# Kernel tuning notes

Measured on AMD Instinct MI355X. Metric: run time of the kernel, lower is better.

## Reference

```python
import jax, jax.numpy as jnp
import numpy as np

NEG = -1e30  # effective -inf that stays stable in fp32 log-sum-exp
BLANK = 0


def _lse3(a, b, c):
    m = jnp.maximum(jnp.maximum(a, b), c)
    return m + jnp.log(jnp.exp(a - m) + jnp.exp(b - m) + jnp.exp(c - m))


def _ctc_loss_sum(log_probs, input_lengths, targets, target_lengths):
    # log_probs: [B, T, V] already log-softmaxed; targets: [B, S] int, blank=0
    B, T, V = log_probs.shape
    S = targets.shape[1]
    L = 2 * S + 1  # extended label seq: blank-interleaved

    ext = jnp.full((B, L), BLANK, dtype=targets.dtype)
    ext = ext.at[:, 1::2].set(targets)  # [B, L]

    # gather per-frame log-probs of extended labels: [B, T, L]
    lp_ext = jnp.take_along_axis(
        log_probs, jnp.broadcast_to(ext[:, None, :], (B, T, L)), axis=2)

    # skip transition s-2 -> s allowed iff ext[s] != blank and ext[s] != ext[s-2]
    ext_prev2 = jnp.pad(ext[:, :-2], ((0, 0), (2, 0)), constant_values=BLANK)
    can_skip = (ext != BLANK) & (ext != ext_prev2) & (jnp.arange(L)[None, :] >= 2)

    # alpha init at t=0
    alpha = jnp.full((B, L), NEG, dtype=log_probs.dtype)
    alpha = alpha.at[:, 0].set(lp_ext[:, 0, 0])
    alpha = alpha.at[:, 1].set(lp_ext[:, 0, 1])

    lp_seq = jnp.swapaxes(lp_ext, 0, 1)[1:]          # [T-1, B, L]
    valid = jnp.arange(1, T)[:, None] < input_lengths[None, :]  # [T-1, B]

    def step(a, xs):
        lp_t, v = xs  # [B, L], [B]
        a1 = jnp.pad(a[:, :-1], ((0, 0), (1, 0)), constant_values=NEG)
        a2 = jnp.pad(a[:, :-2], ((0, 0), (2, 0)), constant_values=NEG)
        a2 = jnp.where(can_skip, a2, NEG)
        new = _lse3(a, a1, a2) + lp_t
        a = jnp.where(v[:, None], new, a)  # freeze past each utterance's length
        return a, None

    alpha, _ = jax.lax.scan(step, alpha, (lp_seq, valid))

    # terminal states: last blank (2*tl) and last label (2*tl - 1)
    end = 2 * target_lengths.astype(jnp.int32)
    aT = jnp.take_along_axis(alpha, jnp.stack([end, end - 1], axis=1), axis=1)  # [B, 2]
    ll = jax.scipy.special.logsumexp(aT, axis=1)
    loss = -ll
    loss = jnp.where(loss > 1e29, 0.0, loss)  # zero_infinity=True
    return jnp.sum(loss)  # reduction='sum'


def setup_inputs() -> dict:
    B, T, V, S = 64, 1024, 512, 128
    key = jax.random.key(0)
    k1, k2, k3, k4 = jax.random.split(key, 4)
    output_tensor = jax.random.normal(k1, (B, T, V), dtype=jnp.float32)
    output_lengths = jax.random.randint(k2, (B,), T // 2, T + 1, dtype=jnp.int32)
    target_tensor = jax.random.randint(k3, (B, S), 1, V, dtype=jnp.int32)  # no blanks
    target_lengths = jax.random.randint(k4, (B,), S // 2, S + 1, dtype=jnp.int32)
    return {"output_tensor": output_tensor, "output_lengths": output_lengths,
            "target_tensor": target_tensor, "target_lengths": target_lengths}


def reference(output_tensor, output_lengths, target_tensor, target_lengths):
    log_probs = jax.nn.log_softmax(output_tensor, axis=2)
    return _ctc_loss_sum(log_probs, output_lengths, target_tensor, target_lengths)
```

## Files before the change

kernel.cpp:

```cpp
#include <hip/hip_runtime.h>
#include <cstdint>

#define T_LEN 1024
#define V_DIM 512
#define S_LEN 128
#define NEG2  (-1.0e30f)
#define CH    32

__device__ float2 g_plab[(size_t)64 * T_LEN * 64 + 64];
__device__ float  g_pblank[(size_t)64 * T_LEN + 64];

static __device__ __forceinline__ void dma16(const void* g, void* l) {
    __builtin_amdgcn_global_load_lds(
        (const __attribute__((address_space(1))) unsigned int*)g,
        (__attribute__((address_space(3))) unsigned int*)l,
        16, 0, 0);
}

static __device__ __forceinline__ float dpp_shr1_f(float x) {
    return __int_as_float(__builtin_amdgcn_update_dpp(
        0, __float_as_int(x), 0x138, 0xF, 0xF, true));
}
static __device__ __forceinline__ int dpp_shr1_i(int x) {
    return __builtin_amdgcn_update_dpp(0, x, 0x138, 0xF, 0xF, true);
}
template <int CTRL>
static __device__ __forceinline__ float dpp_add(float x) {
    const int y = __builtin_amdgcn_update_dpp(0, __float_as_int(x), CTRL, 0xF, 0xF, true);
    return x + __int_as_float(y);
}

__global__ __launch_bounds__(256) void ctc_prep(
    const float* __restrict__ x, const int* __restrict__ lens,
    const int* __restrict__ tgts)
{
    const int lane = threadIdx.x & 63;
    const int wid  = (int)((blockIdx.x * blockDim.x + threadIdx.x) >> 6);
    const int b = wid >> 10;
    const int t = wid & (T_LEN - 1);
    if (t >= lens[b]) return;

    const float* row = x + (size_t)wid * V_DIM;
    const float4 u = *(const float4*)(row + lane * 8);
    const float4 v = *(const float4*)(row + lane * 8 + 4);

    const float L2E = 1.44269504088896340736f;
    float s = exp2f(u.x * L2E) + exp2f(u.y * L2E)
            + exp2f(u.z * L2E) + exp2f(u.w * L2E)
            + exp2f(v.x * L2E) + exp2f(v.y * L2E)
            + exp2f(v.z * L2E) + exp2f(v.w * L2E);
    s = dpp_add<0x111>(s);
    s = dpp_add<0x112>(s);
    s = dpp_add<0x114>(s);
    s = dpp_add<0x118>(s);
    s = dpp_add<0x142>(s);
    s = dpp_add<0x143>(s);
    const float off =
        log2f(__int_as_float(__builtin_amdgcn_readlane(__float_as_int(s), 63)));

    if (lane == 0) g_pblank[wid] = exp2f(u.x * L2E - off);

    const int2 tg = *(const int2*)(tgts + b * S_LEN + 2 * lane);
    g_plab[(size_t)wid * 64 + lane] =
        make_float2(exp2f(row[tg.x] * L2E - off), exp2f(row[tg.y] * L2E - off));
}

struct AlphaState { float a0, a1, a2, a3, a4; int C; };

static __device__ __forceinline__ void alpha_step(
    AlphaState& st, float pb, float2 lp, bool cs1, bool cs3, bool dead)
{
    const float p3 = dpp_shr1_f(st.a3);
    const int   Cp = dpp_shr1_i(st.C);
    const int   Cn = dead ? Cp : st.C;
    int e = 127 + (Cp - Cn);
    e = e < 0 ? 0 : (e > 252 ? 252 : e);
    const float adj = __int_as_float((unsigned)e << 23);
    const float p3v = p3 * adj;
    const float n0 = (st.a0 + p3v) * pb;
    const float n1 = ((st.a1 + st.a0) + (cs1 ? p3v : 0.f)) * lp.x;
    const float n2 = (st.a2 + st.a1) * pb;
    const float n3 = ((st.a3 + st.a2) + (cs3 ? st.a1 : 0.f)) * lp.y;
    const float n4 = (st.a4 + st.a3) * pb;
    st.a0 = n0; st.a1 = n1; st.a2 = n2; st.a3 = n3; st.a4 = n4; st.C = Cn;
}

static __device__ __forceinline__ void alpha_rescale(AlphaState& st)
{
    const float mx = fmaxf(fmaxf(fmaxf(st.a0, st.a1), fmaxf(st.a2, st.a3)), st.a4);
    const int ee = (__float_as_int(mx) >> 23) & 255;
    const bool ok = (ee > 0) && (ee < 255);
    const float sc = ok ? __int_as_float((unsigned)(254 - ee) << 23) : 1.0f;
    const int dC = ok ? (ee - 127) : 0;
    st.a0 *= sc; st.a1 *= sc; st.a2 *= sc; st.a3 *= sc; st.a4 *= sc; st.C += dC;
}

__global__ __launch_bounds__(64) void ctc_alpha(
    const int* __restrict__ lens, const int* __restrict__ tgts,
    const int* __restrict__ tlens, float* __restrict__ out)
{
    __shared__ alignas(16) float lds_pbs[T_LEN];
    __shared__ float2 lds_pl[2][CH * 64];

    const int b    = blockIdx.x;
    const int lane = threadIdx.x;
    const int len  = lens[b];
    const int tl   = tlens[b];
    const int lenm1 = len - 1;

    const int tA = tgts[b * S_LEN + 2 * lane];
    const int tB = tgts[b * S_LEN + 2 * lane + 1];
    const int tPrev = __shfl_up(tB, 1);
    const bool cs1 = (lane > 0) && (tA != tPrev);
    const bool cs3 = (tB != tA);

    const int repOwn = ((lane > 0 && tA == tPrev) ? 1 : 0) + ((tB == tA) ? 1 : 0);
    int ps = repOwn;
    #pragma unroll
    for (int d = 1; d < 64; d <<= 1) {
        const int y = __shfl_up(ps, d);
        if (lane >= d) ps += y;
    }
    const int deadline = 2 * lane + (ps - repOwn);

    const size_t rowb = (size_t)b * T_LEN;
    const float*  __restrict__ pb_b = g_pblank + rowb;
    const float2* __restrict__ pl_b = g_plab + rowb * 64;

    #pragma unroll
    for (int j = 0; j < CH / 2; ++j) {
        const int r = 1 + 2 * j;
        dma16(pl_b + (size_t)r * 64 + lane * 2, &lds_pl[0][j * 128]);
    }

    #pragma unroll
    for (int k = 0; k < T_LEN / 64; ++k)
        lds_pbs[k * 64 + lane] = pb_b[k * 64 + lane + 1];

    AlphaState st;
    st.a0 = 0.f; st.a1 = 0.f; st.a2 = 0.f; st.a3 = 0.f; st.a4 = 0.f; st.C = 0;
    if (lane == 0) { st.a0 = pb_b[0]; st.a1 = pl_b[0].x; }

    int buf = 0;
    int t0 = 1;
    for (; t0 + CH <= len; t0 += CH) {
        float4 pbq[CH / 4];
        #pragma unroll
        for (int j = 0; j < CH / 4; ++j)
            pbq[j] = *(const float4*)&lds_pbs[(t0 - 1) + 4 * j];
        const float* pbr = (const float*)pbq;

        __builtin_amdgcn_s_waitcnt(0x0F70);
        float2 pl[CH];
        #pragma unroll
        for (int i = 0; i < CH; ++i)
            pl[i] = lds_pl[buf][i * 64 + lane];
        #pragma unroll
        for (int j = 0; j < CH / 2; ++j) {
            int r = t0 + CH + 2 * j;
            r = (r < lenm1) ? r : lenm1;
            dma16(pl_b + (size_t)r * 64 + lane * 2, &lds_pl[buf ^ 1][j * 128]);
        }
        #pragma unroll
        for (int i = 0; i < CH; ++i) {
            const bool dead = (deadline >= t0 + i);
            alpha_step(st, pbr[i], pl[i], cs1, cs3, dead);
            if ((i & 3) == 3) alpha_rescale(st);
        }
        buf ^= 1;
    }
    __builtin_amdgcn_s_waitcnt(0x0F70);
    for (int i = 0; t0 + i < len; ++i) {
        const float2 plv = lds_pl[buf][i * 64 + lane];
        const float  pb  = lds_pbs[t0 + i - 1];
        const bool dead = (deadline >= t0 + i);
        alpha_step(st, pb, plv, cs1, cs3, dead);
        if ((i & 3) == 3) alpha_rescale(st);
    }

    const int end = 2 * tl;
    float v1, v2; int C1, C2;
    {
        int s = end;
        int lsrc = s >> 2; if (lsrc > 63) lsrc = 63;
        const int slot = s & 3;
        float cand = (slot == 0) ? st.a0 : (slot == 1) ? st.a1
                   : (slot == 2) ? st.a2 : st.a3;
        if (s == 256) cand = st.a4;
        v1 = __shfl(cand, lsrc);
        C1 = __shfl(st.C, lsrc);

        s = end - 1;
        lsrc = s >> 2;
        const int slot2 = s & 3;
        cand = (slot2 == 0) ? st.a0 : (slot2 == 1) ? st.a1
             : (slot2 == 2) ? st.a2 : st.a3;
        v2 = __shfl(cand, lsrc);
        C2 = __shfl(st.C, lsrc);
    }
    const float l1 = (v1 > 0.f) ? log2f(v1) + (float)C1 : NEG2;
    const float l2 = (v2 > 0.f) ? log2f(v2) + (float)C2 : NEG2;
    const float mM = fmaxf(l1, l2);
    const float ll2 = mM + log2f(exp2f(l1 - mM) + exp2f(l2 - mM));
    float loss = -ll2 * 0.69314718055994530942f;
    if (!(loss < 1e29f)) loss = 0.f;
    if (lane == 0) atomicAdd(out, loss);
}

extern "C" void kernel_launch(void* const* d_in, const int* in_sizes, int n_in,
                              void* d_out, int out_size, void* d_ws, size_t ws_size,
                              hipStream_t stream) {
    const float* x     = (const float*)d_in[0];
    const int*   lens  = (const int*)d_in[1];
    const int*   tgts  = (const int*)d_in[2];
    const int*   tlens = (const int*)d_in[3];
    float* out = (float*)d_out;

    (void)hipMemsetAsync(d_out, 0, (size_t)out_size * sizeof(float), stream);
    ctc_prep<<<(64 * T_LEN) / 4, 256, 0, stream>>>(x, lens, tgts);
    ctc_alpha<<<64, 64, 0, stream>>>(lens, tgts, tlens, out);
}
```

Baseline: 258.4 us.

## Triple-buffer label-prob prefetch and use FMA with float skip masks

Moves the per-chunk label-probability DMA from double to triple buffering, prefetching two chunks ahead. The waitcnt now allows one chunk's loads (16 ops) to stay in flight, so the serial alpha recurrence waits less on global memory latency. It also turns the boolean skip selects into float masks folded into FMAs, which shortens the per-step dependency chain. The cost is more LDS per block and a prologue prefetch of rows 33..63 that does not clamp to the utterance length.

After: 258.2 us. No clear change (-0.1%).

```diff
diff --git a/kernel.cpp b/kernel.cpp
--- a/kernel.cpp
+++ b/kernel.cpp
@@ -68,7 +68,7 @@
 struct AlphaState { float a0, a1, a2, a3, a4; int C; };
 
 static __device__ __forceinline__ void alpha_step(
-    AlphaState& st, float pb, float2 lp, bool cs1, bool cs3, bool dead)
+    AlphaState& st, float pb, float2 lp, float cs1f, float cs3f, bool dead)
 {
     const float p3 = dpp_shr1_f(st.a3);
     const int   Cp = dpp_shr1_i(st.C);
@@ -77,11 +77,13 @@
     e = e < 0 ? 0 : (e > 252 ? 252 : e);
     const float adj = __int_as_float((unsigned)e << 23);
     const float p3v = p3 * adj;
+    const float s01 = st.a0 + st.a1;
+    const float s23 = st.a2 + st.a3;
     const float n0 = (st.a0 + p3v) * pb;
-    const float n1 = ((st.a1 + st.a0) + (cs1 ? p3v : 0.f)) * lp.x;
-    const float n2 = (st.a2 + st.a1) * pb;
-    const float n3 = ((st.a3 + st.a2) + (cs3 ? st.a1 : 0.f)) * lp.y;
-    const float n4 = (st.a4 + st.a3) * pb;
+    const float n1 = fmaf(p3v, cs1f, s01) * lp.x;
+    const float n2 = (st.a1 + st.a2) * pb;
+    const float n3 = fmaf(st.a1, cs3f, s23) * lp.y;
+    const float n4 = (st.a3 + st.a4) * pb;
     st.a0 = n0; st.a1 = n1; st.a2 = n2; st.a3 = n3; st.a4 = n4; st.C = Cn;
 }
 
@@ -100,7 +102,7 @@
     const int* __restrict__ tlens, float* __restrict__ out)
 {
     __shared__ alignas(16) float lds_pbs[T_LEN];
-    __shared__ float2 lds_pl[2][CH * 64];
+    __shared__ float2 lds_pl[3][CH * 64];
 
     const int b    = blockIdx.x;
     const int lane = threadIdx.x;
@@ -113,6 +115,8 @@
     const int tPrev = __shfl_up(tB, 1);
     const bool cs1 = (lane > 0) && (tA != tPrev);
     const bool cs3 = (tB != tA);
+    const float cs1f = cs1 ? 1.0f : 0.0f;
+    const float cs3f = cs3 ? 1.0f : 0.0f;
 
     const int repOwn = ((lane > 0 && tA == tPrev) ? 1 : 0) + ((tB == tA) ? 1 : 0);
     int ps = repOwn;
@@ -128,10 +132,11 @@
     const float2* __restrict__ pl_b = g_plab + rowb * 64;
 
     #pragma unroll
-    for (int j = 0; j < CH / 2; ++j) {
-        const int r = 1 + 2 * j;
-        dma16(pl_b + (size_t)r * 64 + lane * 2, &lds_pl[0][j * 128]);
-    }
+    for (int j = 0; j < CH / 2; ++j)
+        dma16(pl_b + (size_t)(1 + 2 * j) * 64 + lane * 2, &lds_pl[0][j * 128]);
+    #pragma unroll
+    for (int j = 0; j < CH / 2; ++j)
+        dma16(pl_b + (size_t)(33 + 2 * j) * 64 + lane * 2, &lds_pl[1][j * 128]);
 
     #pragma unroll
     for (int k = 0; k < T_LEN / 64; ++k)
@@ -141,40 +146,40 @@
     st.a0 = 0.f; st.a1 = 0.f; st.a2 = 0.f; st.a3 = 0.f; st.a4 = 0.f; st.C = 0;
     if (lane == 0) { st.a0 = pb_b[0]; st.a1 = pl_b[0].x; }
 
-    int buf = 0;
+    int cur = 0;
     int t0 = 1;
     for (; t0 + CH <= len; t0 += CH) {
+        __builtin_amdgcn_s_waitcnt(0x4F70);
         float4 pbq[CH / 4];
         #pragma unroll
         for (int j = 0; j < CH / 4; ++j)
             pbq[j] = *(const float4*)&lds_pbs[(t0 - 1) + 4 * j];
         const float* pbr = (const float*)pbq;
-
-        __builtin_amdgcn_s_waitcnt(0x0F70);
         float2 pl[CH];
         #pragma unroll
         for (int i = 0; i < CH; ++i)
-            pl[i] = lds_pl[buf][i * 64 + lane];
+            pl[i] = lds_pl[cur][i * 64 + lane];
+        int fill = cur + 2; if (fill >= 3) fill -= 3;
         #pragma unroll
         for (int j = 0; j < CH / 2; ++j) {
-            int r = t0 + CH + 2 * j;
+            int r = t0 + 2 * CH + 2 * j;
             r = (r < lenm1) ? r : lenm1;
-            dma16(pl_b + (size_t)r * 64 + lane * 2, &lds_pl[buf ^ 1][j * 128]);
+            dma16(pl_b + (size_t)r * 64 + lane * 2, &lds_pl[fill][j * 128]);
         }
         #pragma unroll
         for (int i = 0; i < CH; ++i) {
             const bool dead = (deadline >= t0 + i);
-            alpha_step(st, pbr[i], pl[i], cs1, cs3, dead);
+            alpha_step(st, pbr[i], pl[i], cs1f, cs3f, dead);
             if ((i & 3) == 3) alpha_rescale(st);
         }
-        buf ^= 1;
+        cur = (cur == 2) ? 0 : cur + 1;
     }
     __builtin_amdgcn_s_waitcnt(0x0F70);
     for (int i = 0; t0 + i < len; ++i) {
-        const float2 plv = lds_pl[buf][i * 64 + lane];
+        const float2 plv = lds_pl[cur][i * 64 + lane];
         const float  pb  = lds_pbs[t0 + i - 1];
         const bool dead = (deadline >= t0 + i);
-        alpha_step(st, pb, plv, cs1, cs3, dead);
+        alpha_step(st, pb, plv, cs1f, cs3f, dead);
         if ((i & 3) == 3) alpha_rescale(st);
     }
 
```
